# Kernel optimization log

Measured on AMD Instinct MI355X. Metric: run time of the kernel, lower is better.

## Reference

```python
import jax, jax.numpy as jnp
import numpy as np

PRUNING_THRESHOLD = 0.02


def setup_inputs() -> dict:
    key = jax.random.key(0)
    ks = jax.random.split(key, 9)
    B, T, D = 2, 2048, 512
    H, S = 8, 16
    hd = D // H
    x = jax.random.normal(ks[0], (B, T, D), dtype=jnp.float32)
    Wqkv = jax.random.normal(ks[1], (3 * D, D), dtype=jnp.float32) * 0.02
    Wout = jax.random.normal(ks[2], (D, D), dtype=jnp.float32) * 0.02
    splat_centers = jax.random.normal(ks[3], (H, S, hd), dtype=jnp.float32) * 0.3
    splat_deltas = jax.random.normal(ks[4], (H, S, hd), dtype=jnp.float32) * 0.05
    splat_log_scales = jax.random.normal(ks[5], (H, S), dtype=jnp.float32) * 0.2 + jnp.float32(np.log(0.5))
    splat_log_amplitudes = jax.random.normal(ks[6], (H, S), dtype=jnp.float32) * 0.1 - 0.5
    movement_scale = jnp.float32(0.08)
    temperature = jnp.float32(1.0)
    return {"x": x, "Wqkv": Wqkv, "Wout": Wout,
            "splat_centers": splat_centers, "splat_deltas": splat_deltas,
            "splat_log_scales": splat_log_scales, "splat_log_amplitudes": splat_log_amplitudes,
            "movement_scale": movement_scale, "temperature": temperature}


def reference(x, Wqkv, Wout, splat_centers, splat_deltas,
              splat_log_scales, splat_log_amplitudes, movement_scale, temperature):
    B, T, D = x.shape
    H, S, hd = splat_centers.shape
    # qkv projection (nn.Linear: y = x @ W.T), split into q,k,v per head
    qkv = (x @ Wqkv.T).reshape(B, T, 3, H, hd)
    q, k, v = qkv[:, :, 0], qkv[:, :, 1], qkv[:, :, 2]  # [B,T,H,hd]
    # effective centers with bounded movement (eval mode: no warmup)
    bounded_scale = jax.nn.sigmoid(movement_scale) * 0.2
    centers = splat_centers + splat_deltas * bounded_scale  # [H,S,hd]
    scales = jnp.clip(jnp.exp(splat_log_scales), 0.01, 2.0)  # [H,S]
    amplitudes = jnp.clip(jnp.exp(splat_log_amplitudes), 1e-06, 10.0)
    amplitudes = amplitudes * (amplitudes > PRUNING_THRESHOLD).astype(amplitudes.dtype)
    # squared distances from tokens to splat centers: [B,T,H,S]
    q_dists = jnp.sum((q[:, :, :, None, :] - centers[None, None]) ** 2, axis=-1)
    k_dists = jnp.sum((k[:, :, :, None, :] - centers[None, None]) ** 2, axis=-1)
    inv_var = 1.0 / (scales ** 2 + 1e-08)  # [H,S]
    q_w = jnp.exp(-0.5 * q_dists * inv_var)  # [B,T,H,S]
    k_w = jnp.exp(-0.5 * k_dists * inv_var)
    # per-head splat-weighted logits: [B,T(query i),T(key j),H]
    logits = jnp.einsum('bihs,bjhs,hs->bijh', q_w, k_w, amplitudes)
    temp = jnp.clip(temperature, 0.1, 10.0)
    # NOTE: original vectorized path softmaxes over dim=1 (query axis) -- faithful
    attn = jax.nn.softmax(logits / temp, axis=1)
    out = jnp.einsum('btjh,bjhd->bthd', attn, v).reshape(B, T, D)
    return out @ Wout.T
```

## Files before the change

### kernel.cpp

```cpp
#include <hip/hip_runtime.h>
#include <hip/hip_bf16.h>
#include <hip/hip_fp16.h>
#include <cstdint>
#include <cstddef>

#define T_SEQ 2048
#define NBATCH 2
#define DIMD 512
#define NH 8
#define NS 16
#define HD 64
#define NBH 16

using s16x8 = __attribute__((ext_vector_type(8))) short;
using f32x4 = __attribute__((ext_vector_type(4))) float;

static __device__ inline unsigned short f2bf(float f) {
  __hip_bfloat16 h = __float2bfloat16(f);
  return reinterpret_cast<unsigned short&>(h);
}
static __device__ inline unsigned short f2h(float f) {
  __half h = __float2half(f);
  return reinterpret_cast<unsigned short&>(h);
}
static __device__ inline float h2f(unsigned short u) {
  __half h = reinterpret_cast<__half&>(u);
  return __half2float(h);
}
static __device__ inline unsigned int pack2(float a, float b) {
  return (unsigned int)f2bf(a) | ((unsigned int)f2bf(b) << 16);
}
static __device__ inline void gload16(const void* g, void* l) {
  __builtin_amdgcn_global_load_lds((const __attribute__((address_space(1))) void*)g,
                                   (__attribute__((address_space(3))) void*)l, 16, 0, 0);
}
static __device__ inline int swz_id() {
  int nwg = gridDim.x * gridDim.y;
  int orig = blockIdx.y * gridDim.x + blockIdx.x;
  return (orig & 7) * (nwg >> 3) + (orig >> 3);
}

static const size_t OFF_VBUF = 0;
static const size_t OFF_AOUT = 2097152;
static const size_t OFF_XH   = 6291456;
static const size_t OFF_XL   = 7340032;
static const size_t OFF_WQH  = 8388608;
static const size_t OFF_WOH  = 9175040;
static const size_t OFF_QABF = 9437184;
static const size_t OFF_KWBF = 9961472;
static const size_t OFF_SPART= 10485760;
static const size_t OFF_VPART= 10616832;
static const size_t OFF_CADJ = 10633216;
static const size_t OFF_IVAR = 10641408;
static const size_t OFF_AMPT = 10641536;

__global__ __launch_bounds__(256) void prep(
    const float* __restrict__ x, const float* __restrict__ Wqkv, const float* __restrict__ Wout,
    const float* __restrict__ centers, const float* __restrict__ deltas,
    const float* __restrict__ lsc, const float* __restrict__ lam,
    const float* __restrict__ ms, const float* __restrict__ tp,
    unsigned short* __restrict__ xh, unsigned short* __restrict__ wqh,
    unsigned short* __restrict__ woh,
    float* __restrict__ cadj, float* __restrict__ ivar, float* __restrict__ ampt) {
  int bid = blockIdx.x;
  int tid = threadIdx.x;
  if (bid == 3072) {
    float bscale = 0.2f / (1.0f + expf(-ms[0]));
    float tclip = fminf(fmaxf(tp[0], 0.1f), 10.0f);
    if (tid < NH * NS) {
      float sc = fminf(fmaxf(expf(lsc[tid]), 0.01f), 2.0f);
      ivar[tid] = 1.0f / (sc * sc + 1e-8f);
      float am = fminf(fmaxf(expf(lam[tid]), 1e-6f), 10.0f);
      am = (am > 0.02f) ? am : 0.0f;
      ampt[tid] = am / tclip;
    }
    for (int e = tid; e < NH * NS * HD; e += 256)
      cadj[e] = centers[e] + deltas[e] * bscale;
    return;
  }
  const float* src; unsigned short* dh; int i4;
  if (bid < 2048)      { src = x;    dh = xh;  i4 = bid * 256 + tid; }
  else if (bid < 2816) { src = Wqkv; dh = wqh; i4 = (bid - 2048) * 256 + tid; }
  else                 { src = Wout; dh = woh; i4 = (bid - 2816) * 256 + tid; }
  float4 v = *(const float4*)&src[(size_t)i4 * 4];
  ushort4 hh;
  hh.x = f2h(v.x); hh.y = f2h(v.y); hh.z = f2h(v.z); hh.w = f2h(v.w);
  *(ushort4*)&dh[(size_t)i4 * 4] = hh;
}

template<int BM, int BN>
__device__ __forceinline__ void gemm_core(
    const unsigned short* Ah, const unsigned short* Bh,
    int K, int m0, int n0,
    unsigned short* ash, unsigned short* bsh,
    f32x4 (&acc)[BM / 32][BN / 32]) {
  constexpr int WM = BM / 2, WN = BN / 2;
  constexpr int MF = WM / 16, NF = WN / 16;
  constexpr int NSA = BM / 8, NSB = BN / 8;
  constexpr int TSEG = NSA + NSB;
  int tid = threadIdx.x;
  int w = tid >> 6, l = tid & 63, lm = l & 15, lq = l >> 4;
  int wm = w >> 1, wn = w & 1;
  int r8 = l >> 3, c8 = l & 7;
  int ksl = (c8 ^ (r8 & 7)) << 3;
#pragma unroll
  for (int mi = 0; mi < MF; ++mi)
#pragma unroll
    for (int ni = 0; ni < NF; ++ni) acc[mi][ni] = (f32x4){0.f, 0.f, 0.f, 0.f};

  for (int k0 = 0; k0 < K; k0 += 64) {
    __syncthreads();
#pragma unroll
    for (int t = 0; t < TSEG / 4; ++t) {
      int s = w + t * 4;
      if (s < NSA) {
        gload16(&Ah[(size_t)(m0 + s * 8 + r8) * K + k0 + ksl], &ash[s * 512]);
      } else {
        int ss = s - NSA;
        gload16(&Bh[(size_t)(n0 + ss * 8 + r8) * K + k0 + ksl], &bsh[ss * 512]);
      }
    }
    __syncthreads();
#pragma unroll
    for (int kh = 0; kh < 2; ++kh) {
      s16x8 fah[MF], fbh[NF];
#pragma unroll
      for (int mi = 0; mi < MF; ++mi) {
        int rr = wm * WM + mi * 16 + lm;
        int off = rr * 64 + ((((kh << 2) | lq) ^ (rr & 7)) << 3);
        fah[mi] = *(const s16x8*)&ash[off];
      }
#pragma unroll
      for (int ni = 0; ni < NF; ++ni) {
        int cc = wn * WN + ni * 16 + lm;
        int off = cc * 64 + ((((kh << 2) | lq) ^ (cc & 7)) << 3);
        fbh[ni] = *(const s16x8*)&bsh[off];
      }
#pragma unroll
      for (int mi = 0; mi < MF; ++mi)
#pragma unroll
        for (int ni = 0; ni < NF; ++ni)
          acc[mi][ni] = __builtin_amdgcn_mfma_f32_16x16x32_f16(fah[mi], fbh[ni], acc[mi][ni], 0, 0, 0);
    }
  }
}

template<int BM, int BN>
__device__ __forceinline__ void write_c(
    float* C, int ldc, int m0, int n0, f32x4 (&acc)[BM / 32][BN / 32]) {
  constexpr int WM = BM / 2, WN = BN / 2;
  int tid = threadIdx.x;
  int w = tid >> 6, l = tid & 63, lm = l & 15, lq = l >> 4;
  int wm = w >> 1, wn = w & 1;
#pragma unroll
  for (int mi = 0; mi < BM / 32; ++mi)
#pragma unroll
    for (int ni = 0; ni < BN / 32; ++ni)
#pragma unroll
      for (int r = 0; r < 4; ++r) {
        int row = m0 + wm * WM + mi * 16 + lq * 4 + r;
        int col = n0 + wn * WN + ni * 16 + lm;
        C[(size_t)row * ldc + col] = acc[mi][ni][r];
      }
}

template<int BM, int BN>
__device__ __forceinline__ void write_ch(
    unsigned short* C, int ldc, int m0, int n0, f32x4 (&acc)[BM / 32][BN / 32]) {
  constexpr int WM = BM / 2, WN = BN / 2;
  int tid = threadIdx.x;
  int w = tid >> 6, l = tid & 63, lm = l & 15, lq = l >> 4;
  int wm = w >> 1, wn = w & 1;
#pragma unroll
  for (int mi = 0; mi < BM / 32; ++mi)
#pragma unroll
    for (int ni = 0; ni < BN / 32; ++ni)
#pragma unroll
      for (int r = 0; r < 4; ++r) {
        int row = m0 + wm * WM + mi * 16 + lq * 4 + r;
        int col = n0 + wn * WN + ni * 16 + lm;
        C[(size_t)row * ldc + col] = f2h(acc[mi][ni][r]);
      }
}

__global__ __launch_bounds__(256) void gemm_qkv(
    const unsigned short* __restrict__ xh, const unsigned short* __restrict__ wqh,
    const float* __restrict__ cadj, const float* __restrict__ ivar,
    const float* __restrict__ ampt, unsigned short* __restrict__ vbuf,
    unsigned short* __restrict__ qa_bf, unsigned short* __restrict__ kw_bf) {
  __shared__ __align__(16) char smem[39168];
  unsigned short* ash = (unsigned short*)smem;
  unsigned short* bsh = (unsigned short*)(smem + 16384);
  int sid = swz_id();
  int bx = sid % 24, by = sid / 24;
  int m0 = by * 128;
  int tid = threadIdx.x;
  f32x4 acc[4][2];
  if (bx >= 16) {
    gemm_core<128, 64>(xh, wqh + (size_t)(1024 + (bx - 16) * 64) * 512,
                       512, m0, 0, ash, bsh, acc);
    write_ch<128, 64>(vbuf, 512, m0, (bx - 16) * 64, acc);
    return;
  }
  bool isk = bx >= 8;
  int h = bx & 7;
  gemm_core<128, 64>(xh, wqh + (size_t)((isk ? 512 : 0) + h * 64) * 512,
                     512, m0, 0, ash, bsh, acc);
  __syncthreads();
  float* q_s = (float*)smem;
  float* c_s = (float*)(smem + 34816);
  {
    int w = tid >> 6, l = tid & 63, lm = l & 15, lq = l >> 4;
    int wm = w >> 1, wn = w & 1;
#pragma unroll
    for (int mi = 0; mi < 4; ++mi)
#pragma unroll
      for (int ni = 0; ni < 2; ++ni)
#pragma unroll
        for (int r = 0; r < 4; ++r)
          q_s[(wm * 64 + mi * 16 + lq * 4 + r) * 68 + wn * 32 + ni * 16 + lm] = acc[mi][ni][r];
    int cr = tid >> 4, d4 = tid & 15;
    *(float4*)&c_s[cr * 68 + d4 * 4] = *(const float4*)&cadj[(h * 16 + cr) * 64 + d4 * 4];
  }
  __syncthreads();
  int s = tid & 15, rbase = tid >> 4;
  float iv = ivar[h * 16 + s];
  float am = ampt[h * 16 + s];
  const float4* crow = (const float4*)&c_s[s * 68];
#pragma unroll
  for (int t = 0; t < 8; ++t) {
    int r = t * 16 + rbase;
    const float4* qrow = (const float4*)&q_s[r * 68];
    float d2 = 0.0f;
#pragma unroll
    for (int d4 = 0; d4 < 16; ++d4) {
      float4 qv = qrow[d4], cv = crow[d4];
      float e0 = qv.x - cv.x, e1 = qv.y - cv.y, e2 = qv.z - cv.z, e3 = qv.w - cv.w;
      d2 = fmaf(e0, e0, d2); d2 = fmaf(e1, e1, d2);
      d2 = fmaf(e2, e2, d2); d2 = fmaf(e3, e3, d2);
    }
    float val = __expf(-0.5f * d2 * iv);
    int row = m0 + r;
    int b = row >> 11, i = row & 2047;
    size_t base = ((size_t)(b * 8 + h) * T_SEQ + i) * 32;
    if (!isk) {
      qa_bf[base + s] = f2bf(val * am);
      qa_bf[base + 16 + s] = 0;
    } else {
      int xorv = (r >> 1) & 3;
      int slot = s >> 3, e = s & 7;
      kw_bf[base + (size_t)((slot ^ xorv) << 3) + e] = f2bf(val);
      kw_bf[base + (size_t)(((2 + slot) ^ xorv) << 3) + e] = 0;
    }
  }
}

__global__ __launch_bounds__(256) void gemm_out(
    const unsigned short* __restrict__ aout_h, const unsigned short* __restrict__ woh,
    float* __restrict__ out) {
  __shared__ __align__(16) unsigned short ash[64 * 64];
  __shared__ __align__(16) unsigned short bsh[64 * 64];
  int sid = swz_id();
  int bx = sid % 8, by = sid / 8;
  f32x4 acc[2][2];
  gemm_core<64, 64>(aout_h + (size_t)by * 64 * 512, woh + (size_t)bx * 64 * 512,
                    512, 0, 0, ash, bsh, acc);
  write_c<64, 64>(out, 512, by * 64, bx * 64, acc);
}

__global__ __launch_bounds__(256) void k3_colsum(
    const unsigned short* __restrict__ qa_bf, const unsigned short* __restrict__ kw_bf,
    float* __restrict__ spart) {
  int sid = swz_id();
  int jblk = sid & 15, yy = sid >> 4;
  int bh = yy >> 2, iq = yy & 3;
  int tid = threadIdx.x;
  int w = tid >> 6, l = tid & 63, lm = l & 15, lq = l >> 4;
  int jbase = (jblk << 7) + (w << 5);
  int sw = lq ^ ((lm >> 1) & 3);
  size_t base32 = (size_t)bh * T_SEQ * 32;
  s16x8 kwB0 = *(const s16x8*)&kw_bf[base32 + (size_t)(jbase + lm) * 32 + sw * 8];
  s16x8 kwB1 = *(const s16x8*)&kw_bf[base32 + (size_t)(jbase + 16 + lm) * 32 + sw * 8];
  const unsigned short* qp = qa_bf + base32 + ((size_t)(iq * 512) + lm) * 32 + lq * 8;
  float s0 = 0.0f, s1 = 0.0f;
  f32x4 z = (f32x4){0.f, 0.f, 0.f, 0.f};
#pragma unroll 4
  for (int it = 0; it < 512; it += 16) {
    s16x8 qaA = *(const s16x8*)(qp + (size_t)it * 32);
    f32x4 L0 = __builtin_amdgcn_mfma_f32_16x16x32_bf16(qaA, kwB0, z, 0, 0, 0);
    f32x4 L1 = __builtin_amdgcn_mfma_f32_16x16x32_bf16(qaA, kwB1, z, 0, 0, 0);
    s0 += (__expf(L0[0]) - 1.0f) + (__expf(L0[1]) - 1.0f)
        + (__expf(L0[2]) - 1.0f) + (__expf(L0[3]) - 1.0f);
    s1 += (__expf(L1[0]) - 1.0f) + (__expf(L1[1]) - 1.0f)
        + (__expf(L1[2]) - 1.0f) + (__expf(L1[3]) - 1.0f);
  }
  s0 += __shfl_xor(s0, 16); s0 += __shfl_xor(s0, 32);
  s1 += __shfl_xor(s1, 16); s1 += __shfl_xor(s1, 32);
  if (l < 16) {
    float* sp = spart + ((size_t)iq * NBH + bh) * T_SEQ;
    sp[jbase + lm] = s0;
    sp[jbase + 16 + lm] = s1;
  }
}

__global__ __launch_bounds__(256) void k3c_vt(
    const unsigned short* __restrict__ vbuf, const float* __restrict__ spart,
    unsigned short* __restrict__ vt, float* __restrict__ vpart) {
  int bh = blockIdx.y; int b = bh >> 3, h = bh & 7;
  int js = blockIdx.x << 7;
  int tid = threadIdx.x;
  __shared__ unsigned short t_s[64][136];
  __shared__ float red[16][64];
  int jg = tid >> 4, dq = tid & 15;
  const unsigned short* vb = vbuf + (size_t)b * T_SEQ * 512 + h * 64;
  const float* sp0 = spart + (size_t)bh * T_SEQ + js;
  const float* sp1 = spart + ((size_t)NBH + bh) * T_SEQ + js;
  const float* sp2 = spart + ((size_t)2 * NBH + bh) * T_SEQ + js;
  const float* sp3 = spart + ((size_t)3 * NBH + bh) * T_SEQ + js;
  float a0 = 0.f, a1 = 0.f, a2 = 0.f, a3 = 0.f;
#pragma unroll
  for (int p = 0; p < 8; ++p) {
    int j = p * 16 + jg;
    float s = 1.0f / (2048.0f + sp0[j] + sp1[j] + sp2[j] + sp3[j]);
    ushort4 vu = *(const ushort4*)&vb[(size_t)(js + j) * 512 + dq * 4];
    float v0 = h2f(vu.x) * s, v1 = h2f(vu.y) * s, v2 = h2f(vu.z) * s, v3 = h2f(vu.w) * s;
    t_s[dq * 4 + 0][j] = f2bf(v0);
    t_s[dq * 4 + 1][j] = f2bf(v1);
    t_s[dq * 4 + 2][j] = f2bf(v2);
    t_s[dq * 4 + 3][j] = f2bf(v3);
    a0 += v0; a1 += v1; a2 += v2; a3 += v3;
  }
  red[jg][dq * 4 + 0] = a0; red[jg][dq * 4 + 1] = a1;
  red[jg][dq * 4 + 2] = a2; red[jg][dq * 4 + 3] = a3;
  __syncthreads();
  if (tid < 64) {
    float t = 0.f;
#pragma unroll
    for (int g = 0; g < 16; ++g) t += red[g][tid];
    vpart[((size_t)blockIdx.x * NBH + bh) * 64 + tid] = t;
  }
#pragma unroll
  for (int p = 0; p < 4; ++p) {
    int idx = p * 256 + tid;
    int d = idx >> 4, seg = idx & 15;
    int4 val = *(const int4*)&t_s[d][seg * 8];
    int col = ((seg >> 3) << 6) + ((((seg & 7) ^ (d & 7))) << 3);
    *(int4*)&vt[(size_t)bh * 131072 + (size_t)d * 2048 + js + col] = val;
  }
}

__global__ __launch_bounds__(512) void k4_attnout(
    const unsigned short* __restrict__ qa_bf, const unsigned short* __restrict__ kw_bf,
    const unsigned short* __restrict__ vt, const float* __restrict__ vpart,
    unsigned short* __restrict__ aout_h) {
  int sid = swz_id();
  int bh = sid >> 5; int b = bh >> 3, h = bh & 7;
  int i0 = (sid & 31) << 6;
  int tid = threadIdx.x;
  int w = tid >> 6, l = tid & 63, lm = l & 15, lq = l >> 4;
  int g = w >> 1, jh = w & 1;
  __shared__ __align__(16) unsigned short kwS[2][2][2048];
  __shared__ __align__(16) unsigned short vtS[2][2][4096];
  __shared__ __align__(16) unsigned short pss[8][2][640];
  const unsigned short* kwg = kw_bf + (size_t)bh * (T_SEQ * 32) + (size_t)jh * (1024 * 32);
  const unsigned short* vtg = vt + (size_t)bh * 131072 + jh * 1024;
  int swk = lq ^ ((lm >> 1) & 3);
  int swv = lm & 7;
  s16x8 qaB = *(const s16x8*)&qa_bf[((size_t)bh * T_SEQ + i0 + g * 16 + lm) * 32 + lq * 8];
  f32x4 acc0 = (f32x4){0.f,0.f,0.f,0.f}, acc1 = acc0, acc2 = acc0, acc3 = acc0;
  f32x4 z = (f32x4){0.f, 0.f, 0.f, 0.f};

  auto stage = [&](int c, int bsel) {
#pragma unroll
    for (int t = 0; t < 2; ++t) {
      int li = g * 2 + t;
      gload16(&vtg[(size_t)(li * 8 + (l >> 3)) * 2048 + c * 64 + (l & 7) * 8],
              &vtS[jh][bsel][li * 512]);
    }
    gload16(&kwg[(size_t)(c * 64 + g * 16 + (l >> 2)) * 32 + (l & 3) * 8],
            &kwS[jh][bsel][g * 512]);
  };

  stage(0, 0);
  __syncthreads();
  for (int c = 0; c < 16; ++c) {
    int bsel = c & 1;
    if (c < 15) stage(c + 1, bsel ^ 1);
    const unsigned short* kwb = kwS[jh][bsel];
    const unsigned short* vtb = vtS[jh][bsel];
#pragma unroll
    for (int s = 0; s < 2; ++s) {
      s16x8 ka0 = *(const s16x8*)&kwb[(s * 32 + lm) * 32 + swk * 8];
      s16x8 ka1 = *(const s16x8*)&kwb[(s * 32 + 16 + lm) * 32 + swk * 8];
      s16x8 vb0 = *(const s16x8*)&vtb[(size_t)(0 + lm) * 64 + (((4 * s + lq) ^ swv) << 3)];
      s16x8 vb1 = *(const s16x8*)&vtb[(size_t)(16 + lm) * 64 + (((4 * s + lq) ^ swv) << 3)];
      s16x8 vb2 = *(const s16x8*)&vtb[(size_t)(32 + lm) * 64 + (((4 * s + lq) ^ swv) << 3)];
      s16x8 vb3 = *(const s16x8*)&vtb[(size_t)(48 + lm) * 64 + (((4 * s + lq) ^ swv) << 3)];
      f32x4 L0 = __builtin_amdgcn_mfma_f32_16x16x32_bf16(ka0, qaB, z, 0, 0, 0);
      f32x4 L1 = __builtin_amdgcn_mfma_f32_16x16x32_bf16(ka1, qaB, z, 0, 0, 0);
      uint2 u01, u23;
      u01.x = pack2(__expf(L0[0]) - 1.0f, __expf(L0[1]) - 1.0f);
      u01.y = pack2(__expf(L0[2]) - 1.0f, __expf(L0[3]) - 1.0f);
      u23.x = pack2(__expf(L1[0]) - 1.0f, __expf(L1[1]) - 1.0f);
      u23.y = pack2(__expf(L1[2]) - 1.0f, __expf(L1[3]) - 1.0f);
      unsigned short* prow = &pss[w][s][lm * 40];
      *(uint2*)&prow[lq * 4] = u01;
      *(uint2*)&prow[16 + lq * 4] = u23;
      s16x8 pA = *(const s16x8*)&prow[lq * 8];
      __builtin_amdgcn_s_setprio(1);
      acc0 = __builtin_amdgcn_mfma_f32_16x16x32_bf16(pA, vb0, acc0, 0, 0, 0);
      acc1 = __builtin_amdgcn_mfma_f32_16x16x32_bf16(pA, vb1, acc1, 0, 0, 0);
      acc2 = __builtin_amdgcn_mfma_f32_16x16x32_bf16(pA, vb2, acc2, 0, 0, 0);
      acc3 = __builtin_amdgcn_mfma_f32_16x16x32_bf16(pA, vb3, acc3, 0, 0, 0);
      __builtin_amdgcn_s_setprio(0);
    }
    __syncthreads();
  }
  f32x4 accs[4] = {acc0, acc1, acc2, acc3};
  float* mrg = (float*)&vtS[0][0][0];
  if (jh == 1) {
#pragma unroll
    for (int df = 0; df < 4; ++df)
#pragma unroll
      for (int r = 0; r < 4; ++r)
        mrg[((g * 4 + df) * 4 + r) * 64 + l] = accs[df][r];
  }
  __syncthreads();
  if (jh == 0) {
#pragma unroll
    for (int df = 0; df < 4; ++df) {
      int d = df * 16 + lm;
      float vs = 0.0f;
#pragma unroll
      for (int js = 0; js < 16; ++js) vs += vpart[((size_t)js * NBH + bh) * 64 + d];
#pragma unroll
      for (int r = 0; r < 4; ++r) {
        int row = i0 + g * 16 + lq * 4 + r;
        float o = accs[df][r] + mrg[((g * 4 + df) * 4 + r) * 64 + l] + vs;
        aout_h[((size_t)b * T_SEQ + row) * DIMD + h * 64 + d] = f2h(o);
      }
    }
  }
}

extern "C" void kernel_launch(void* const* d_in, const int* in_sizes, int n_in,
                              void* d_out, int out_size, void* d_ws, size_t ws_size,
                              hipStream_t stream) {
  const float* x    = (const float*)d_in[0];
  const float* Wqkv = (const float*)d_in[1];
  const float* Wout = (const float*)d_in[2];
  const float* ctr  = (const float*)d_in[3];
  const float* dlt  = (const float*)d_in[4];
  const float* lsc  = (const float*)d_in[5];
  const float* lam  = (const float*)d_in[6];
  const float* ms   = (const float*)d_in[7];
  const float* tp   = (const float*)d_in[8];
  float* ws = (float*)d_ws;
  unsigned short* vbuf   = (unsigned short*)(ws + OFF_VBUF);
  unsigned short* aout_h = (unsigned short*)(ws + OFF_AOUT);
  unsigned short* xh  = (unsigned short*)(ws + OFF_XH);
  unsigned short* wqh = (unsigned short*)(ws + OFF_WQH);
  unsigned short* woh = (unsigned short*)(ws + OFF_WOH);
  unsigned short* qa_bf = (unsigned short*)(ws + OFF_QABF);
  unsigned short* kw_bf = (unsigned short*)(ws + OFF_KWBF);
  float* spart = ws + OFF_SPART;
  float* vpart = ws + OFF_VPART;
  float* cadj  = ws + OFF_CADJ;
  float* ivar  = ws + OFF_IVAR;
  float* ampt  = ws + OFF_AMPT;
  unsigned short* vt = xh;
  float* out = (float*)d_out;

  prep<<<3073, 256, 0, stream>>>(x, Wqkv, Wout, ctr, dlt, lsc, lam, ms, tp,
                                 xh, wqh, woh, cadj, ivar, ampt);
  gemm_qkv<<<dim3(24, 32), 256, 0, stream>>>(xh, wqh, cadj, ivar, ampt,
                                             vbuf, qa_bf, kw_bf);
  k3_colsum<<<dim3(16, 64), 256, 0, stream>>>(qa_bf, kw_bf, spart);
  k3c_vt<<<dim3(16, 16), 256, 0, stream>>>(vbuf, spart, vt, vpart);
  k4_attnout<<<dim3(32, 16), 512, 0, stream>>>(qa_bf, kw_bf, vt, vpart, aout_h);
  gemm_out<<<dim3(8, 64), 256, 0, stream>>>(aout_h, woh, out);
}
```

Measured before the change: 83.32 us.

## Double query rows per attention block and keep probabilities in registers

The attention-output kernel now handles 128 query rows per block instead of 64, with each wave computing two 16-row fragments. This halves the grid and reuses each staged K/V tile across twice as many queries. The K-tile read order is permuted so the logit MFMA output layout matches the A-operand layout of the PV MFMA. That lets the exp'd probabilities be packed straight into registers instead of going through a shared-memory round trip. It costs more accumulator registers and leaves fewer blocks (256) to fill the CUs.

```diff
diff --git a/kernel.cpp b/kernel.cpp
--- a/kernel.cpp
+++ b/kernel.cpp
@@ -43,7 +43,6 @@
 static const size_t OFF_VBUF = 0;
 static const size_t OFF_AOUT = 2097152;
 static const size_t OFF_XH   = 6291456;
-static const size_t OFF_XL   = 7340032;
 static const size_t OFF_WQH  = 8388608;
 static const size_t OFF_WOH  = 9175040;
 static const size_t OFF_QABF = 9437184;
@@ -354,31 +353,37 @@
     const unsigned short* __restrict__ vt, const float* __restrict__ vpart,
     unsigned short* __restrict__ aout_h) {
   int sid = swz_id();
-  int bh = sid >> 5; int b = bh >> 3, h = bh & 7;
-  int i0 = (sid & 31) << 6;
+  int bh = sid >> 4; int b = bh >> 3, h = bh & 7;
+  int i0 = (sid & 15) << 7;
   int tid = threadIdx.x;
   int w = tid >> 6, l = tid & 63, lm = l & 15, lq = l >> 4;
-  int g = w >> 1, jh = w & 1;
+  int ig = w >> 1, jh = w & 1;
   __shared__ __align__(16) unsigned short kwS[2][2][2048];
   __shared__ __align__(16) unsigned short vtS[2][2][4096];
-  __shared__ __align__(16) unsigned short pss[8][2][640];
   const unsigned short* kwg = kw_bf + (size_t)bh * (T_SEQ * 32) + (size_t)jh * (1024 * 32);
   const unsigned short* vtg = vt + (size_t)bh * 131072 + jh * 1024;
-  int swk = lq ^ ((lm >> 1) & 3);
+  int p0 = ((lm >> 2) << 3) | (lm & 3);
+  int sw0 = lq ^ ((lm >> 1) & 1);
+  int sw1 = sw0 ^ 2;
   int swv = lm & 7;
-  s16x8 qaB = *(const s16x8*)&qa_bf[((size_t)bh * T_SEQ + i0 + g * 16 + lm) * 32 + lq * 8];
-  f32x4 acc0 = (f32x4){0.f,0.f,0.f,0.f}, acc1 = acc0, acc2 = acc0, acc3 = acc0;
+  s16x8 qaB0 = *(const s16x8*)&qa_bf[((size_t)bh * T_SEQ + i0 + ig * 32 + lm) * 32 + lq * 8];
+  s16x8 qaB1 = *(const s16x8*)&qa_bf[((size_t)bh * T_SEQ + i0 + ig * 32 + 16 + lm) * 32 + lq * 8];
+  f32x4 acc[2][4];
+#pragma unroll
+  for (int ifr = 0; ifr < 2; ++ifr)
+#pragma unroll
+    for (int df = 0; df < 4; ++df) acc[ifr][df] = (f32x4){0.f, 0.f, 0.f, 0.f};
   f32x4 z = (f32x4){0.f, 0.f, 0.f, 0.f};
 
   auto stage = [&](int c, int bsel) {
 #pragma unroll
     for (int t = 0; t < 2; ++t) {
-      int li = g * 2 + t;
+      int li = ig * 2 + t;
       gload16(&vtg[(size_t)(li * 8 + (l >> 3)) * 2048 + c * 64 + (l & 7) * 8],
               &vtS[jh][bsel][li * 512]);
     }
-    gload16(&kwg[(size_t)(c * 64 + g * 16 + (l >> 2)) * 32 + (l & 3) * 8],
-            &kwS[jh][bsel][g * 512]);
+    gload16(&kwg[(size_t)(c * 64 + ig * 16 + (l >> 2)) * 32 + (l & 3) * 8],
+            &kwS[jh][bsel][ig * 512]);
   };
 
   stage(0, 0);
@@ -390,56 +395,60 @@
     const unsigned short* vtb = vtS[jh][bsel];
 #pragma unroll
     for (int s = 0; s < 2; ++s) {
-      s16x8 ka0 = *(const s16x8*)&kwb[(s * 32 + lm) * 32 + swk * 8];
-      s16x8 ka1 = *(const s16x8*)&kwb[(s * 32 + 16 + lm) * 32 + swk * 8];
+      s16x8 ka0 = *(const s16x8*)&kwb[(s * 32 + p0) * 32 + sw0 * 8];
+      s16x8 ka1 = *(const s16x8*)&kwb[(s * 32 + p0 + 4) * 32 + sw1 * 8];
       s16x8 vb0 = *(const s16x8*)&vtb[(size_t)(0 + lm) * 64 + (((4 * s + lq) ^ swv) << 3)];
       s16x8 vb1 = *(const s16x8*)&vtb[(size_t)(16 + lm) * 64 + (((4 * s + lq) ^ swv) << 3)];
       s16x8 vb2 = *(const s16x8*)&vtb[(size_t)(32 + lm) * 64 + (((4 * s + lq) ^ swv) << 3)];
       s16x8 vb3 = *(const s16x8*)&vtb[(size_t)(48 + lm) * 64 + (((4 * s + lq) ^ swv) << 3)];
-      f32x4 L0 = __builtin_amdgcn_mfma_f32_16x16x32_bf16(ka0, qaB, z, 0, 0, 0);
-      f32x4 L1 = __builtin_amdgcn_mfma_f32_16x16x32_bf16(ka1, qaB, z, 0, 0, 0);
-      uint2 u01, u23;
-      u01.x = pack2(__expf(L0[0]) - 1.0f, __expf(L0[1]) - 1.0f);
-      u01.y = pack2(__expf(L0[2]) - 1.0f, __expf(L0[3]) - 1.0f);
-      u23.x = pack2(__expf(L1[0]) - 1.0f, __expf(L1[1]) - 1.0f);
-      u23.y = pack2(__expf(L1[2]) - 1.0f, __expf(L1[3]) - 1.0f);
-      unsigned short* prow = &pss[w][s][lm * 40];
-      *(uint2*)&prow[lq * 4] = u01;
-      *(uint2*)&prow[16 + lq * 4] = u23;
-      s16x8 pA = *(const s16x8*)&prow[lq * 8];
-      __builtin_amdgcn_s_setprio(1);
-      acc0 = __builtin_amdgcn_mfma_f32_16x16x32_bf16(pA, vb0, acc0, 0, 0, 0);
-      acc1 = __builtin_amdgcn_mfma_f32_16x16x32_bf16(pA, vb1, acc1, 0, 0, 0);
-      acc2 = __builtin_amdgcn_mfma_f32_16x16x32_bf16(pA, vb2, acc2, 0, 0, 0);
-      acc3 = __builtin_amdgcn_mfma_f32_16x16x32_bf16(pA, vb3, acc3, 0, 0, 0);
-      __builtin_amdgcn_s_setprio(0);
+#pragma unroll
+      for (int ifr = 0; ifr < 2; ++ifr) {
+        s16x8 qaB = ifr ? qaB1 : qaB0;
+        f32x4 L0 = __builtin_amdgcn_mfma_f32_16x16x32_bf16(ka0, qaB, z, 0, 0, 0);
+        f32x4 L1 = __builtin_amdgcn_mfma_f32_16x16x32_bf16(ka1, qaB, z, 0, 0, 0);
+        union { unsigned int u4[4]; s16x8 v; } cvt;
+        cvt.u4[0] = pack2(__expf(L0[0]) - 1.0f, __expf(L0[1]) - 1.0f);
+        cvt.u4[1] = pack2(__expf(L0[2]) - 1.0f, __expf(L0[3]) - 1.0f);
+        cvt.u4[2] = pack2(__expf(L1[0]) - 1.0f, __expf(L1[1]) - 1.0f);
+        cvt.u4[3] = pack2(__expf(L1[2]) - 1.0f, __expf(L1[3]) - 1.0f);
+        s16x8 pA = cvt.v;
+        __builtin_amdgcn_s_setprio(1);
+        acc[ifr][0] = __builtin_amdgcn_mfma_f32_16x16x32_bf16(pA, vb0, acc[ifr][0], 0, 0, 0);
+        acc[ifr][1] = __builtin_amdgcn_mfma_f32_16x16x32_bf16(pA, vb1, acc[ifr][1], 0, 0, 0);
+        acc[ifr][2] = __builtin_amdgcn_mfma_f32_16x16x32_bf16(pA, vb2, acc[ifr][2], 0, 0, 0);
+        acc[ifr][3] = __builtin_amdgcn_mfma_f32_16x16x32_bf16(pA, vb3, acc[ifr][3], 0, 0, 0);
+        __builtin_amdgcn_s_setprio(0);
+      }
     }
     __syncthreads();
   }
-  f32x4 accs[4] = {acc0, acc1, acc2, acc3};
   float* mrg = (float*)&vtS[0][0][0];
   if (jh == 1) {
 #pragma unroll
-    for (int df = 0; df < 4; ++df)
-#pragma unroll
-      for (int r = 0; r < 4; ++r)
-        mrg[((g * 4 + df) * 4 + r) * 64 + l] = accs[df][r];
+    for (int ifr = 0; ifr < 2; ++ifr)
+#pragma unroll
+      for (int df = 0; df < 4; ++df)
+#pragma unroll
+        for (int r = 0; r < 4; ++r)
+          mrg[(((ig * 2 + ifr) * 4 + df) * 4 + r) * 64 + l] = acc[ifr][df][r];
   }
   __syncthreads();
   if (jh == 0) {
 #pragma unroll
-    for (int df = 0; df < 4; ++df) {
-      int d = df * 16 + lm;
-      float vs = 0.0f;
-#pragma unroll
-      for (int js = 0; js < 16; ++js) vs += vpart[((size_t)js * NBH + bh) * 64 + d];
-#pragma unroll
-      for (int r = 0; r < 4; ++r) {
-        int row = i0 + g * 16 + lq * 4 + r;
-        float o = accs[df][r] + mrg[((g * 4 + df) * 4 + r) * 64 + l] + vs;
-        aout_h[((size_t)b * T_SEQ + row) * DIMD + h * 64 + d] = f2h(o);
-      }
-    }
+    for (int ifr = 0; ifr < 2; ++ifr)
+#pragma unroll
+      for (int df = 0; df < 4; ++df) {
+        int d = df * 16 + lm;
+        float vs = 0.0f;
+#pragma unroll
+        for (int js = 0; js < 16; ++js) vs += vpart[((size_t)js * NBH + bh) * 64 + d];
+#pragma unroll
+        for (int r = 0; r < 4; ++r) {
+          int row = i0 + ig * 32 + ifr * 16 + lq * 4 + r;
+          float o = acc[ifr][df][r] + mrg[(((ig * 2 + ifr) * 4 + df) * 4 + r) * 64 + l] + vs;
+          aout_h[((size_t)b * T_SEQ + row) * DIMD + h * 64 + d] = f2h(o);
+        }
+      }
   }
 }
 
@@ -477,6 +486,6 @@
                                              vbuf, qa_bf, kw_bf);
   k3_colsum<<<dim3(16, 64), 256, 0, stream>>>(qa_bf, kw_bf, spart);
   k3c_vt<<<dim3(16, 16), 256, 0, stream>>>(vbuf, spart, vt, vpart);
-  k4_attnout<<<dim3(32, 16), 512, 0, stream>>>(qa_bf, kw_bf, vt, vpart, aout_h);
+  k4_attnout<<<dim3(16, 16), 512, 0, stream>>>(qa_bf, kw_bf, vt, vpart, aout_h);
   gemm_out<<<dim3(8, 64), 256, 0, stream>>>(aout_h, woh, out);
 }
```

After: 84.11 us. No clear change (+1.0%).
